# Performance work log

Measured on AMD Instinct MI355X. Metric: run time of the kernel, lower is better.

Reference implementation:

```python
import jax, jax.numpy as jnp
import numpy as np

B, S, I, H, O = 64, 2048, 128, 256, 128


def setup_inputs() -> dict:
    key = jax.random.key(0)
    ks = jax.random.split(key, 7)
    s = 1.0 / np.sqrt(H)
    return {
        "x": jax.random.normal(ks[0], (B, S, I), dtype=jnp.float32),
        "W_ih": jax.random.uniform(ks[1], (H, I), jnp.float32, -s, s),
        "W_hh": jax.random.uniform(ks[2], (H, H), jnp.float32, -s, s),
        "b_ih": jax.random.uniform(ks[3], (H,), jnp.float32, -s, s),
        "b_hh": jax.random.uniform(ks[4], (H,), jnp.float32, -s, s),
        "W_fc": jax.random.uniform(ks[5], (O, H), jnp.float32, -s, s),
        "b_fc": jax.random.uniform(ks[6], (O,), jnp.float32, -s, s),
    }


def reference(x, W_ih, W_hh, b_ih, b_hh, W_fc, b_fc):
    # h_t = tanh(x_t @ W_ih^T + h_{t-1} @ W_hh^T + b_ih + b_hh)
    b = b_ih + b_hh
    # Precompute input projection for all timesteps in one GEMM: [B,S,H]
    xproj = jnp.einsum('bsi,hi->bsh', x, W_ih) + b

    def step(h, xp_t):  # h: [B,H], xp_t: [B,H]
        h_next = jnp.tanh(xp_t + h @ W_hh.T)
        return h_next, h_next

    h0 = jnp.zeros((B, H), dtype=x.dtype)
    _, hs = jax.lax.scan(step, h0, jnp.swapaxes(xproj, 0, 1))  # hs: [S,B,H]
    hidden_states = jnp.swapaxes(hs, 0, 1)  # [B,S,H]
    outputs = jnp.einsum('bsh,oh->bso', hidden_states, W_fc) + b_fc  # [B,S,O]
    return outputs, hidden_states
```

## Files before the change

kernel.cpp:

```cpp
#include <hip/hip_runtime.h>

#define BB 64
#define SS 2048
#define II 128
#define HH 256
#define OO 128

typedef _Float16 h2_t __attribute__((ext_vector_type(2)));

__device__ __forceinline__ h2_t u2h(unsigned u) {
    union { unsigned u; h2_t h; } c; c.u = u; return c.h;
}

#if __has_builtin(__builtin_amdgcn_fdot2)
__device__ __forceinline__ float fdot2(unsigned h, unsigned w, float acc) {
    return __builtin_amdgcn_fdot2(u2h(h), u2h(w), acc, false);
}
#else
__device__ __forceinline__ float fdot2(unsigned h, unsigned w, float acc) {
    h2_t hh = u2h(h), ww = u2h(w);
    acc = fmaf((float)hh.x, (float)ww.x, acc);
    acc = fmaf((float)hh.y, (float)ww.y, acc);
    return acc;
}
#endif

__global__ void prep_kernel(const float* __restrict__ W_ih, const float* __restrict__ b_ih,
                            const float* __restrict__ b_hh, const float* __restrict__ W_fc,
                            float* __restrict__ wihT, float* __restrict__ wfcT,
                            float* __restrict__ biasc, unsigned* __restrict__ wsw,
                            const float* __restrict__ W_hh) {
    int idx = blockIdx.x * 256 + threadIdx.x;
    if (idx < HH * II) {
        int j = idx / II, k = idx % II;
        wihT[k * HH + j] = W_ih[idx];
    }
    if (idx < OO * HH) {
        int j = idx / HH, k = idx % HH;
        wfcT[k * OO + j] = W_fc[idx];
    }
    if (idx < HH * (HH / 2)) {
        int d   = idx & 3;
        int s   = idx >> 2;
        int l   = s & 63;
        int rem = s >> 6;
        int i    = rem & 7;
        int pair = (rem >> 3) & 1;
        int w    = rem >> 4;
        int j    = w * 32 + (l & 15) * 2 + pair;
        int word = (l >> 4) * 32 + i * 4 + d;
        union { h2_t h; unsigned u; } pk;
        pk.h.x = (_Float16)W_hh[j * HH + 2 * word];
        pk.h.y = (_Float16)W_hh[j * HH + 2 * word + 1];
        wsw[idx] = pk.u;
    }
    if (idx < HH) biasc[idx] = b_ih[idx] + b_hh[idx];
}

template<int KD, int JD, int RT>
__global__ __launch_bounds__(256, 2)
void gemm_rk(const float* __restrict__ A, const float* __restrict__ Wt,
             const float* __restrict__ bias, float* __restrict__ C) {
    constexpr int KT = 64;
    constexpr int TJ = JD / 8;
    constexpr int TR = RT / 8;
    static_assert(TJ * TR == 256, "bad tiling");

    __shared__ __align__(16) float a_lds[RT][KT];
    __shared__ __align__(16) float w_lds[KT][JD];

    const int tid = threadIdx.x;
    const int tj = tid % TJ;
    const int tr = tid / TJ;
    const long r0 = (long)blockIdx.x * RT;

    float acc[8][8];
#pragma unroll
    for (int r = 0; r < 8; ++r)
#pragma unroll
        for (int j = 0; j < 8; ++j) acc[r][j] = 0.0f;

    for (int kt = 0; kt < KD; kt += KT) {
        {
            constexpr int NF4 = RT * KT / 4;
#pragma unroll
            for (int f = 0; f < NF4 / 256; ++f) {
                int fl = f * 256 + tid;
                int rr = fl / (KT / 4), kk4 = fl % (KT / 4);
                *(float4*)&a_lds[rr][kk4 * 4] =
                    *(const float4*)&A[(r0 + rr) * KD + kt + kk4 * 4];
            }
        }
        {
            constexpr int NF4 = KT * JD / 4;
#pragma unroll
            for (int f = 0; f < NF4 / 256; ++f) {
                int fl = f * 256 + tid;
                int kk = fl / (JD / 4), jj4 = fl % (JD / 4);
                *(float4*)&w_lds[kk][jj4 * 4] =
                    *(const float4*)&Wt[(long)(kt + kk) * JD + jj4 * 4];
            }
        }
        __syncthreads();

#pragma unroll 4
        for (int k4 = 0; k4 < KT; k4 += 4) {
            float4 xv[8];
#pragma unroll
            for (int r = 0; r < 8; ++r)
                xv[r] = *(const float4*)&a_lds[tr * 8 + r][k4];
#pragma unroll
            for (int i = 0; i < 4; ++i) {
                float4 wa = *(const float4*)&w_lds[k4 + i][tj * 8];
                float4 wb = *(const float4*)&w_lds[k4 + i][tj * 8 + 4];
#pragma unroll
                for (int r = 0; r < 8; ++r) {
                    float xs = (i == 0) ? xv[r].x : (i == 1) ? xv[r].y
                             : (i == 2) ? xv[r].z : xv[r].w;
                    acc[r][0] = fmaf(xs, wa.x, acc[r][0]);
                    acc[r][1] = fmaf(xs, wa.y, acc[r][1]);
                    acc[r][2] = fmaf(xs, wa.z, acc[r][2]);
                    acc[r][3] = fmaf(xs, wa.w, acc[r][3]);
                    acc[r][4] = fmaf(xs, wb.x, acc[r][4]);
                    acc[r][5] = fmaf(xs, wb.y, acc[r][5]);
                    acc[r][6] = fmaf(xs, wb.z, acc[r][6]);
                    acc[r][7] = fmaf(xs, wb.w, acc[r][7]);
                }
            }
        }
        __syncthreads();
    }

    float4 b0 = *(const float4*)&bias[tj * 8];
    float4 b1 = *(const float4*)&bias[tj * 8 + 4];
#pragma unroll
    for (int r = 0; r < 8; ++r) {
        long row = r0 + tr * 8 + r;
        float4 o0, o1;
        o0.x = acc[r][0] + b0.x; o0.y = acc[r][1] + b0.y;
        o0.z = acc[r][2] + b0.z; o0.w = acc[r][3] + b0.w;
        o1.x = acc[r][4] + b1.x; o1.y = acc[r][5] + b1.y;
        o1.z = acc[r][6] + b1.z; o1.w = acc[r][7] + b1.w;
        *(float4*)&C[row * JD + tj * 8]     = o0;
        *(float4*)&C[row * JD + tj * 8 + 4] = o1;
    }
}

__global__ __attribute__((amdgpu_waves_per_eu(2, 2))) __launch_bounds__(512)
void rnn_scan(const unsigned* __restrict__ wsw, float* __restrict__ hid) {
    const int b   = blockIdx.x;
    const int tid = threadIdx.x;
    const int w   = tid >> 6;
    const int l   = tid & 63;
    const int sl  = l & 15;
    const int q   = l >> 4;

    const int j0 = w * 32 + sl * 2;

    __shared__ __align__(16) unsigned h16[2][4 * 36];

    const uint4* __restrict__ wp = (const uint4*)wsw + ((size_t)w << 10) + l;

    for (int i = tid; i < 2 * 4 * 36; i += 512) ((unsigned*)h16)[i] = 0u;

    float* __restrict__ base = hid + (size_t)b * SS * HH;
    float2 xp0 = *(const float2*)&base[j0];
    float2 xp1 = *(const float2*)&base[HH + j0];
    __syncthreads();

#pragma unroll 1
    for (int t = 0; t < SS; ++t) {
        uint4 wA[8], wB[8];
#pragma unroll
        for (int i = 0; i < 8; ++i) {
            wA[i] = wp[i * 64];
            wB[i] = wp[(8 + i) * 64];
        }

        float2 xp2 = make_float2(0.f, 0.f);
        if (t + 2 < SS) xp2 = *(const float2*)&base[(size_t)(t + 2) * HH + j0];

        const uint4* hb = (const uint4*)&h16[t & 1][q * 36];
        float aA0 = 0.f, aA1 = 0.f, aB0 = 0.f, aB1 = 0.f;
#pragma unroll
        for (int i = 0; i < 8; ++i) {
            uint4 hv = hb[i];
            aA0 = fdot2(hv.x, wA[i].x, aA0);
            aA1 = fdot2(hv.y, wA[i].y, aA1);
            aA0 = fdot2(hv.z, wA[i].z, aA0);
            aA1 = fdot2(hv.w, wA[i].w, aA1);
            aB0 = fdot2(hv.x, wB[i].x, aB0);
            aB1 = fdot2(hv.y, wB[i].y, aB1);
            aB0 = fdot2(hv.z, wB[i].z, aB0);
            aB1 = fdot2(hv.w, wB[i].w, aB1);
        }
        float sA = aA0 + aA1;
        float sB = aB0 + aB1;
        sA += __shfl_xor(sA, 16, 64);
        sA += __shfl_xor(sA, 32, 64);
        sB += __shfl_xor(sB, 16, 64);
        sB += __shfl_xor(sB, 32, 64);

        float s0 = xp0.x + sA;
        float s1 = xp0.y + sB;
        float e0  = __expf(2.0f * s0);
        float e1  = __expf(2.0f * s1);
        float hn0 = 1.0f - __fdividef(2.0f, e0 + 1.0f);
        float hn1 = 1.0f - __fdividef(2.0f, e1 + 1.0f);

        if (q == 0) {
            union { h2_t h; unsigned u; } pk;
            pk.h.x = (_Float16)hn0;
            pk.h.y = (_Float16)hn1;
            const int W = j0 >> 1;
            h16[(t & 1) ^ 1][(W >> 5) * 36 + (W & 31)] = pk.u;
            *(float2*)&base[(size_t)t * HH + j0] = make_float2(hn0, hn1);
        }
        __syncthreads();
        xp0 = xp1;
        xp1 = xp2;
    }
}

extern "C" void kernel_launch(void* const* d_in, const int* in_sizes, int n_in,
                              void* d_out, int out_size, void* d_ws, size_t ws_size,
                              hipStream_t stream) {
    const float* x    = (const float*)d_in[0];
    const float* W_ih = (const float*)d_in[1];
    const float* W_hh = (const float*)d_in[2];
    const float* b_ih = (const float*)d_in[3];
    const float* b_hh = (const float*)d_in[4];
    const float* W_fc = (const float*)d_in[5];
    const float* b_fc = (const float*)d_in[6];

    float* out_fc  = (float*)d_out;
    float* hidden  = (float*)d_out + (size_t)BB * SS * OO;

    float*    wihT  = (float*)d_ws;
    float*    wfcT  = wihT + II * HH;
    float*    biasc = wfcT + HH * OO;
    unsigned* wsw   = (unsigned*)(biasc + HH);

    const long NR = (long)BB * SS;

    prep_kernel<<<128, 256, 0, stream>>>(W_ih, b_ih, b_hh, W_fc,
                                         wihT, wfcT, biasc, wsw, W_hh);
    gemm_rk<II, HH, 64><<<NR / 64, 256, 0, stream>>>(x, wihT, biasc, hidden);
    rnn_scan<<<BB, 512, 0, stream>>>(wsw, hidden);
    gemm_rk<HH, OO, 128><<<NR / 128, 256, 0, stream>>>(hidden, wfcT, b_fc, out_fc);
}
```

Measured before the change: 1.456 ms.

## Repartition RNN scan so each lane computes four outputs over shorter K slices

```diff
diff --git a/kernel.cpp b/kernel.cpp
--- a/kernel.cpp
+++ b/kernel.cpp
@@ -40,18 +40,20 @@
         wfcT[k * OO + j] = W_fc[idx];
     }
     if (idx < HH * (HH / 2)) {
-        int d   = idx & 3;
-        int s   = idx >> 2;
-        int l   = s & 63;
-        int rem = s >> 6;
-        int i    = rem & 7;
-        int pair = (rem >> 3) & 1;
-        int w    = rem >> 4;
-        int j    = w * 32 + (l & 15) * 2 + pair;
-        int word = (l >> 4) * 32 + i * 4 + d;
+        int d  = idx & 3;
+        int s  = idx >> 2;
+        int l  = s & 63;
+        int i  = (s >> 6) & 15;
+        int w  = s >> 10;
+        int o  = i >> 2;
+        int kk = i & 3;
+        int sl = l & 7;
+        int q  = l >> 3;
+        int j  = w * 32 + sl * 4 + o;
+        int kb = q * 32 + kk * 8 + d * 2;
         union { h2_t h; unsigned u; } pk;
-        pk.h.x = (_Float16)W_hh[j * HH + 2 * word];
-        pk.h.y = (_Float16)W_hh[j * HH + 2 * word + 1];
+        pk.h.x = (_Float16)W_hh[j * HH + kb];
+        pk.h.y = (_Float16)W_hh[j * HH + kb + 1];
         wsw[idx] = pk.u;
     }
     if (idx < HH) biasc[idx] = b_ih[idx] + b_hh[idx];
@@ -152,69 +154,83 @@
     const int tid = threadIdx.x;
     const int w   = tid >> 6;
     const int l   = tid & 63;
-    const int sl  = l & 15;
-    const int q   = l >> 4;
-
-    const int j0 = w * 32 + sl * 2;
-
-    __shared__ __align__(16) unsigned h16[2][4 * 36];
-
-    const uint4* __restrict__ wp = (const uint4*)wsw + ((size_t)w << 10) + l;
-
-    for (int i = tid; i < 2 * 4 * 36; i += 512) ((unsigned*)h16)[i] = 0u;
+    const int sl  = l & 7;
+    const int q   = l >> 3;
+    const int g   = q >> 1;
+
+    const int jown = w * 32 + sl * 4 + g;
+
+    __shared__ __align__(16) _Float16 h16[2][8 * 40];
+
+    const uint4* __restrict__ wp0 = (const uint4*)wsw + ((size_t)w << 10) + l;
+    const uint4* __restrict__ wp1 = wp0 + 256;
+    const uint4* __restrict__ wp2 = wp0 + 512;
+    const uint4* __restrict__ wp3 = wp0 + 768;
+
+    for (int i = tid; i < 2 * 320 / 2; i += 512) ((unsigned*)h16)[i] = 0u;
 
     float* __restrict__ base = hid + (size_t)b * SS * HH;
-    float2 xp0 = *(const float2*)&base[j0];
-    float2 xp1 = *(const float2*)&base[HH + j0];
+    float xp0 = base[jown];
+    float xp1 = base[HH + jown];
     __syncthreads();
 
 #pragma unroll 1
     for (int t = 0; t < SS; ++t) {
-        uint4 wA[8], wB[8];
-#pragma unroll
-        for (int i = 0; i < 8; ++i) {
-            wA[i] = wp[i * 64];
-            wB[i] = wp[(8 + i) * 64];
-        }
-
-        float2 xp2 = make_float2(0.f, 0.f);
-        if (t + 2 < SS) xp2 = *(const float2*)&base[(size_t)(t + 2) * HH + j0];
-
-        const uint4* hb = (const uint4*)&h16[t & 1][q * 36];
-        float aA0 = 0.f, aA1 = 0.f, aB0 = 0.f, aB1 = 0.f;
-#pragma unroll
-        for (int i = 0; i < 8; ++i) {
-            uint4 hv = hb[i];
-            aA0 = fdot2(hv.x, wA[i].x, aA0);
-            aA1 = fdot2(hv.y, wA[i].y, aA1);
-            aA0 = fdot2(hv.z, wA[i].z, aA0);
-            aA1 = fdot2(hv.w, wA[i].w, aA1);
-            aB0 = fdot2(hv.x, wB[i].x, aB0);
-            aB1 = fdot2(hv.y, wB[i].y, aB1);
-            aB0 = fdot2(hv.z, wB[i].z, aB0);
-            aB1 = fdot2(hv.w, wB[i].w, aB1);
-        }
-        float sA = aA0 + aA1;
-        float sB = aB0 + aB1;
-        sA += __shfl_xor(sA, 16, 64);
-        sA += __shfl_xor(sA, 32, 64);
-        sB += __shfl_xor(sB, 16, 64);
-        sB += __shfl_xor(sB, 32, 64);
-
-        float s0 = xp0.x + sA;
-        float s1 = xp0.y + sB;
-        float e0  = __expf(2.0f * s0);
-        float e1  = __expf(2.0f * s1);
-        float hn0 = 1.0f - __fdividef(2.0f, e0 + 1.0f);
-        float hn1 = 1.0f - __fdividef(2.0f, e1 + 1.0f);
-
-        if (q == 0) {
-            union { h2_t h; unsigned u; } pk;
-            pk.h.x = (_Float16)hn0;
-            pk.h.y = (_Float16)hn1;
-            const int W = j0 >> 1;
-            h16[(t & 1) ^ 1][(W >> 5) * 36 + (W & 31)] = pk.u;
-            *(float2*)&base[(size_t)t * HH + j0] = make_float2(hn0, hn1);
+        uint4 w0[4], w1[4], w2[4], w3[4];
+#pragma unroll
+        for (int kk = 0; kk < 4; ++kk) {
+            w0[kk] = wp0[kk * 64];
+            w1[kk] = wp1[kk * 64];
+            w2[kk] = wp2[kk * 64];
+            w3[kk] = wp3[kk * 64];
+        }
+
+        const int t2 = (t + 2 < SS) ? (t + 2) : (SS - 1);
+        float xp2 = base[(size_t)t2 * HH + jown];
+
+        const uint4* hb = (const uint4*)&h16[t & 1][q * 40];
+        float p0 = 0.f, p1 = 0.f, p2 = 0.f, p3 = 0.f;
+#pragma unroll
+        for (int kk = 0; kk < 4; ++kk) {
+            uint4 hv = hb[kk];
+            p0 = fdot2(hv.x, w0[kk].x, p0);
+            p0 = fdot2(hv.y, w0[kk].y, p0);
+            p0 = fdot2(hv.z, w0[kk].z, p0);
+            p0 = fdot2(hv.w, w0[kk].w, p0);
+            p1 = fdot2(hv.x, w1[kk].x, p1);
+            p1 = fdot2(hv.y, w1[kk].y, p1);
+            p1 = fdot2(hv.z, w1[kk].z, p1);
+            p1 = fdot2(hv.w, w1[kk].w, p1);
+            p2 = fdot2(hv.x, w2[kk].x, p2);
+            p2 = fdot2(hv.y, w2[kk].y, p2);
+            p2 = fdot2(hv.z, w2[kk].z, p2);
+            p2 = fdot2(hv.w, w2[kk].w, p2);
+            p3 = fdot2(hv.x, w3[kk].x, p3);
+            p3 = fdot2(hv.y, w3[kk].y, p3);
+            p3 = fdot2(hv.z, w3[kk].z, p3);
+            p3 = fdot2(hv.w, w3[kk].w, p3);
+        }
+
+        p0 += __shfl_xor(p0, 8, 64);
+        p1 += __shfl_xor(p1, 8, 64);
+        p2 += __shfl_xor(p2, 8, 64);
+        p3 += __shfl_xor(p3, 8, 64);
+
+        float s  = (g == 0) ? p0 : (g == 1) ? p1 : (g == 2) ? p2 : p3;
+        float x1 = (g == 0) ? p1 : (g == 1) ? p0 : (g == 2) ? p3 : p2;
+        s += __shfl_xor(x1, 16, 64);
+        float x2 = (g == 0) ? p2 : (g == 1) ? p3 : (g == 2) ? p0 : p1;
+        s += __shfl_xor(x2, 32, 64);
+        float x3 = (g == 0) ? p3 : (g == 1) ? p2 : (g == 2) ? p1 : p0;
+        s += __shfl_xor(x3, 48, 64);
+
+        s += xp0;
+        float e  = __expf(2.0f * s);
+        float hn = 1.0f - __fdividef(2.0f, e + 1.0f);
+
+        if (!(q & 1)) {
+            h16[(t & 1) ^ 1][(jown >> 5) * 40 + (jown & 31)] = (_Float16)hn;
+            base[(size_t)t * HH + jown] = hn;
         }
         __syncthreads();
         xp0 = xp1;
```

Measured after the change: 1.580 ms. 1.09x slower.
